# Kernel optimization log

Measured on AMD Instinct MI355X. Metric: run time of the kernel, lower is better.

The kernel has to match this reference:

```python
import jax, jax.numpy as jnp
import numpy as np

N_NODES = 100000
N_EDGES = 1600000
IN_DIM, HID, OUT = 128, 128, 64


def setup_inputs() -> dict:
    key = jax.random.key(0)
    ks = jax.random.split(key, 8)
    x = jax.random.normal(ks[0], (N_NODES, IN_DIM), dtype=jnp.float32)
    edge_index = jax.random.randint(ks[1], (2, N_EDGES), 0, N_NODES, dtype=jnp.int64)
    # Glorot-ish init for GCNConv linear weights (stored as [in, out]).
    W1 = jax.random.normal(ks[2], (IN_DIM, HID), dtype=jnp.float32) * (1.0 / np.sqrt(IN_DIM))
    b1 = jnp.zeros((HID,), dtype=jnp.float32)
    W2 = jax.random.normal(ks[3], (HID, HID), dtype=jnp.float32) * (1.0 / np.sqrt(HID))
    b2 = jnp.zeros((HID,), dtype=jnp.float32)
    W3 = jax.random.normal(ks[4], (HID, OUT), dtype=jnp.float32) * (1.0 / np.sqrt(HID))
    b3 = jnp.zeros((OUT,), dtype=jnp.float32)
    return {"x": x, "W1": W1, "b1": b1, "W2": W2, "b2": b2,
            "W3": W3, "b3": b3, "edge_index": edge_index}


def _gcn_norm(edge_index, num_nodes):
    # GCNConv default: add self loops, symmetric normalization D^{-1/2} A D^{-1/2}.
    loops = jnp.arange(num_nodes, dtype=edge_index.dtype)
    src = jnp.concatenate([edge_index[0], loops])
    dst = jnp.concatenate([edge_index[1], loops])
    deg = jax.ops.segment_sum(jnp.ones_like(dst, dtype=jnp.float32), dst,
                              num_segments=num_nodes)
    dinv = jnp.where(deg > 0, jax.lax.rsqrt(deg), 0.0)
    norm = dinv[src] * dinv[dst]  # [E + N]
    return src, dst, norm


def _gcn_conv(h, W, b, src, dst, norm, num_nodes):
    h = h @ W                                   # transform first (PyG GCNConv)
    msg = h[src] * norm[:, None]                # gather + scale
    agg = jax.ops.segment_sum(msg, dst, num_segments=num_nodes)  # scatter-add
    return agg + b


def _dropout(h, key, p=0.5):
    keep = jax.random.bernoulli(key, 1.0 - p, h.shape)
    return jnp.where(keep, h / (1.0 - p), 0.0)


def reference(x, W1, b1, W2, b2, W3, b3, edge_index):
    num_nodes = x.shape[0]
    src, dst, norm = _gcn_norm(edge_index, num_nodes)
    kd1, kd2 = jax.random.split(jax.random.key(42))
    h = jax.nn.relu(_gcn_conv(x, W1, b1, src, dst, norm, num_nodes))
    h = _dropout(h, kd1)
    h = jax.nn.relu(_gcn_conv(h, W2, b2, src, dst, norm, num_nodes))
    h = _dropout(h, kd2)
    return _gcn_conv(h, W3, b3, src, dst, norm, num_nodes)
```

## Files before the change

### kernel.cpp

```cpp
#include <hip/hip_runtime.h>
#include <stdint.h>

#define NN 100000
#define NE 1600000
#define NMASKW 400000
#define HIST_BLKS 6250
#define WSPL_BLKS 20

typedef float f4 __attribute__((ext_vector_type(4)));
typedef float f2 __attribute__((ext_vector_type(2)));
typedef unsigned short us4 __attribute__((ext_vector_type(4)));
typedef short s16x8 __attribute__((ext_vector_type(8)));

__device__ inline float bf2f(unsigned short u) {
  return __uint_as_float(((uint32_t)u) << 16);
}
__device__ inline unsigned short f2bf(float f) {
  uint32_t u = __float_as_uint(f);
  return (unsigned short)((u + 0x7fffu + ((u >> 16) & 1u)) >> 16);
}
__device__ inline float lo16(uint32_t q) { return __uint_as_float(q << 16); }
__device__ inline float hi16(uint32_t q) { return __uint_as_float(q & 0xffff0000u); }

__host__ __device__ inline void threefry2x32(uint32_t k0, uint32_t k1,
                                             uint32_t x0, uint32_t x1,
                                             uint32_t* y0, uint32_t* y1) {
  uint32_t ks[3] = {k0, k1, k0 ^ k1 ^ 0x1BD11BDAu};
  x0 += ks[0]; x1 += ks[1];
  const uint32_t R[2][4] = {{13u, 15u, 26u, 6u}, {17u, 29u, 16u, 24u}};
#pragma unroll
  for (int i = 0; i < 5; ++i) {
#pragma unroll
    for (int j = 0; j < 4; ++j) {
      uint32_t r = R[i & 1][j];
      x0 += x1;
      x1 = (x1 << r) | (x1 >> (32u - r));
      x1 ^= x0;
    }
    x0 += ks[(i + 1) % 3];
    x1 += ks[(i + 2) % 3] + (uint32_t)(i + 1);
  }
  *y0 = x0; *y1 = x1;
}

__device__ inline uint32_t tf_bits32(uint32_t k0, uint32_t k1, uint32_t idx) {
  uint32_t a, b;
  threefry2x32(k0, k1, 0u, idx, &a, &b);
  return a ^ b;
}

__global__ __launch_bounds__(256) void k_histmask(
    const int* __restrict__ ei, uint32_t* __restrict__ cnt,
    int* __restrict__ slot, uint32_t* __restrict__ m1, uint32_t* __restrict__ m2,
    uint32_t k10, uint32_t k11, uint32_t k20, uint32_t k21) {
  int b = blockIdx.x;
  int q = b / 5, r = b % 5;
  if (r < 4) {
    int e = (q * 4 + r) * 256 + threadIdx.x;
    if (e < NE) {
      int d = ei[NE + e];
      slot[e] = (int)atomicAdd(&cnt[d], 1u);
    }
  } else {
    int t = q * 256 + threadIdx.x;
    if (t < NMASKW) {
      uint32_t base = (uint32_t)t * 32u;
      uint32_t w1 = 0, w2 = 0;
#pragma unroll 4
      for (int j = 0; j < 32; ++j) {
        w1 |= (tf_bits32(k10, k11, base + j) >> 31) << j;
        w2 |= (tf_bits32(k20, k21, base + j) >> 31) << j;
      }
      m1[t] = w1;
      m2[t] = w2;
    }
  }
}

__global__ __launch_bounds__(256) void k_scan1(const uint32_t* __restrict__ cnt,
                                               uint32_t* __restrict__ rpp,
                                               uint32_t* __restrict__ bsum,
                                               float* __restrict__ dinv) {
  __shared__ uint32_t sh[256];
  int t = threadIdx.x;
  int base = blockIdx.x * 1024 + t * 4;
  uint32_t v[4];
  uint32_t s = 0;
#pragma unroll
  for (int i = 0; i < 4; ++i) {
    int idx = base + i;
    v[i] = (idx < NN) ? cnt[idx] : 0u;
    if (idx < NN) dinv[idx] = 1.0f / sqrtf((float)(v[i] + 1u));
    s += v[i];
  }
  sh[t] = s;
  __syncthreads();
  for (int off = 1; off < 256; off <<= 1) {
    uint32_t x = sh[t];
    if (t >= off) x += sh[t - off];
    __syncthreads();
    sh[t] = x;
    __syncthreads();
  }
  uint32_t run = (t > 0) ? sh[t - 1] : 0u;
  if (t == 255) bsum[blockIdx.x] = sh[255];
#pragma unroll
  for (int i = 0; i < 4; ++i) {
    int idx = base + i;
    if (idx < NN) rpp[idx] = run;
    run += v[i];
  }
}

__global__ __launch_bounds__(128) void k_scan2(const uint32_t* __restrict__ bsum,
                                               uint32_t* __restrict__ bsumP,
                                               uint32_t* __restrict__ rpp, int nb) {
  __shared__ uint32_t sh[128];
  int t = threadIdx.x;
  uint32_t v = (t < nb) ? bsum[t] : 0u;
  sh[t] = v;
  __syncthreads();
  for (int off = 1; off < 128; off <<= 1) {
    uint32_t x = sh[t];
    if (t >= off) x += sh[t - off];
    __syncthreads();
    sh[t] = x;
    __syncthreads();
  }
  uint32_t excl = (t > 0) ? sh[t - 1] : 0u;
  if (t < nb) bsumP[t] = excl;
  if (t == nb - 1) rpp[NN] = (uint32_t)NE - excl;
}

__global__ __launch_bounds__(256) void k_scatwsplit(
    const int* __restrict__ ei, const uint32_t* __restrict__ rpp,
    const uint32_t* __restrict__ bsumP,
    const int* __restrict__ slot, const float* __restrict__ dinv,
    uint2* __restrict__ e2,
    const float* __restrict__ W1, const float* __restrict__ W2,
    const float* __restrict__ W3,
    unsigned short* __restrict__ w1h, unsigned short* __restrict__ w1l,
    unsigned short* __restrict__ w2h, unsigned short* __restrict__ w2l,
    unsigned short* __restrict__ w3h, unsigned short* __restrict__ w3l) {
  int b = blockIdx.x;
  if (b < WSPL_BLKS) {
    int bb = b * 4 + (threadIdx.x >> 6);
    int lane = threadIdx.x & 63;
    const float* W; unsigned short *H, *L; int dout, j0;
    if (bb < 32)      { W = W1; H = w1h; L = w1l; dout = 128; j0 = bb; }
    else if (bb < 64) { W = W2; H = w2h; L = w2l; dout = 128; j0 = bb - 32; }
    else              { W = W3; H = w3h; L = w3l; dout = 64;  j0 = bb - 64; }
    int kk = j0 & 3;
    int ct = j0 >> 2;
    int kbase = kk * 32 + (lane >> 4) * 8;
    int col = ct * 16 + (lane & 15);
    us4 h0, h1, l0, l1;
#pragma unroll
    for (int j = 0; j < 4; ++j) {
      float v = W[(size_t)(kbase + j) * dout + col];
      h0[j] = f2bf(v);
      l0[j] = f2bf(v - bf2f(h0[j]));
      float v2 = W[(size_t)(kbase + 4 + j) * dout + col];
      h1[j] = f2bf(v2);
      l1[j] = f2bf(v2 - bf2f(h1[j]));
    }
    size_t o = ((size_t)j0 * 64 + lane) * 8;
    *(us4*)(H + o) = h0; *(us4*)(H + o + 4) = h1;
    *(us4*)(L + o) = l0; *(us4*)(L + o + 4) = l1;
  } else {
    int e = (b - WSPL_BLKS) * 256 + threadIdx.x;
    if (e < NE) {
      int s = ei[e];
      int d = ei[NE + e];
      float w = dinv[s] * dinv[d];
      uint2 rec;
      rec.x = (uint32_t)s;
      rec.y = __float_as_uint(w);
      uint32_t pos = rpp[d] + bsumP[(uint32_t)d >> 10] + (uint32_t)slot[e];
      e2[pos] = rec;
    }
  }
}

__global__ __launch_bounds__(256) void k_gemm1(
    const float* __restrict__ A, const unsigned short* __restrict__ Wh,
    const unsigned short* __restrict__ Wl, unsigned short* __restrict__ C) {
  constexpr int NT = 8;
  const int w = threadIdx.x >> 6;
  const int lane = threadIdx.x & 63;
  const int row0 = blockIdx.x * 128 + w * 32;
  const int aoff = (lane >> 4) * 8;
  s16x8 afh[2][4], afl[2][4];
#pragma unroll
  for (int g = 0; g < 2; ++g) {
    int ar = row0 + g * 16 + (lane & 15);
    if (ar >= NN) ar = NN - 1;
#pragma unroll
    for (int kk = 0; kk < 4; ++kk) {
      f4 v0 = *(const f4*)(A + (size_t)ar * 128 + kk * 32 + aoff);
      f4 v1 = *(const f4*)(A + (size_t)ar * 128 + kk * 32 + aoff + 4);
#pragma unroll
      for (int j = 0; j < 4; ++j) {
        unsigned short h = f2bf(v0[j]);
        afh[g][kk][j] = (short)h;
        afl[g][kk][j] = (short)f2bf(v0[j] - bf2f(h));
        unsigned short h2 = f2bf(v1[j]);
        afh[g][kk][j + 4] = (short)h2;
        afl[g][kk][j + 4] = (short)f2bf(v1[j] - bf2f(h2));
      }
    }
  }
  f4 acc[2][NT];
#pragma unroll
  for (int g = 0; g < 2; ++g)
#pragma unroll
    for (int t = 0; t < NT; ++t) acc[g][t] = (f4){0.f, 0.f, 0.f, 0.f};
#pragma unroll
  for (int ct = 0; ct < NT; ++ct) {
#pragma unroll
    for (int kk = 0; kk < 4; ++kk) {
      size_t bo = ((size_t)(ct * 4 + kk) * 64 + lane) * 8;
      s16x8 bh = *(const s16x8*)(Wh + bo);
      s16x8 bl = *(const s16x8*)(Wl + bo);
#pragma unroll
      for (int g = 0; g < 2; ++g) {
        acc[g][ct] = __builtin_amdgcn_mfma_f32_16x16x32_bf16(afh[g][kk], bh, acc[g][ct], 0, 0, 0);
        acc[g][ct] = __builtin_amdgcn_mfma_f32_16x16x32_bf16(afh[g][kk], bl, acc[g][ct], 0, 0, 0);
        acc[g][ct] = __builtin_amdgcn_mfma_f32_16x16x32_bf16(afl[g][kk], bh, acc[g][ct], 0, 0, 0);
      }
    }
  }
  const int cbase = lane & 15;
#pragma unroll
  for (int g = 0; g < 2; ++g) {
    const int rbase = row0 + g * 16 + (lane >> 4) * 4;
#pragma unroll
    for (int ct = 0; ct < NT; ++ct) {
#pragma unroll
      for (int r = 0; r < 4; ++r) {
        int gr = rbase + r;
        if (gr < NN) C[(size_t)gr * 128 + ct * 16 + cbase] = f2bf(acc[g][ct][r]);
      }
    }
  }
}

template <int DOUT>
__global__ __launch_bounds__(256) void k_gemm_mfma(
    const unsigned short* __restrict__ Ah, const unsigned short* __restrict__ Al,
    const unsigned short* __restrict__ Wh, const unsigned short* __restrict__ Wl,
    unsigned short* __restrict__ C) {
  constexpr int NT = DOUT / 16;
  const int w = threadIdx.x >> 6;
  const int lane = threadIdx.x & 63;
  const int row0 = blockIdx.x * 128 + w * 32;
  const int aoff = (lane >> 4) * 8;
  s16x8 afh[2][4], afl[2][4];
#pragma unroll
  for (int g = 0; g < 2; ++g) {
    int ar = row0 + g * 16 + (lane & 15);
    if (ar >= NN) ar = NN - 1;
#pragma unroll
    for (int kk = 0; kk < 4; ++kk) {
      afh[g][kk] = *(const s16x8*)(Ah + (size_t)ar * 128 + kk * 32 + aoff);
      afl[g][kk] = *(const s16x8*)(Al + (size_t)ar * 128 + kk * 32 + aoff);
    }
  }
  f4 acc[2][NT];
#pragma unroll
  for (int g = 0; g < 2; ++g)
#pragma unroll
    for (int t = 0; t < NT; ++t) acc[g][t] = (f4){0.f, 0.f, 0.f, 0.f};
#pragma unroll
  for (int ct = 0; ct < NT; ++ct) {
#pragma unroll
    for (int kk = 0; kk < 4; ++kk) {
      size_t bo = ((size_t)(ct * 4 + kk) * 64 + lane) * 8;
      s16x8 bh = *(const s16x8*)(Wh + bo);
      s16x8 bl = *(const s16x8*)(Wl + bo);
#pragma unroll
      for (int g = 0; g < 2; ++g) {
        acc[g][ct] = __builtin_amdgcn_mfma_f32_16x16x32_bf16(afh[g][kk], bh, acc[g][ct], 0, 0, 0);
        acc[g][ct] = __builtin_amdgcn_mfma_f32_16x16x32_bf16(afh[g][kk], bl, acc[g][ct], 0, 0, 0);
        acc[g][ct] = __builtin_amdgcn_mfma_f32_16x16x32_bf16(afl[g][kk], bh, acc[g][ct], 0, 0, 0);
      }
    }
  }
  const int cbase = lane & 15;
#pragma unroll
  for (int g = 0; g < 2; ++g) {
    const int rbase = row0 + g * 16 + (lane >> 4) * 4;
#pragma unroll
    for (int ct = 0; ct < NT; ++ct) {
#pragma unroll
      for (int r = 0; r < 4; ++r) {
        int gr = rbase + r;
        if (gr < NN) C[(size_t)gr * DOUT + ct * 16 + cbase] = f2bf(acc[g][ct][r]);
      }
    }
  }
}

__global__ __launch_bounds__(256) void k_agg_mid(
    const unsigned short* __restrict__ hb, const uint32_t* __restrict__ rpp,
    const uint32_t* __restrict__ bsumP,
    const uint2* __restrict__ e2, const float* __restrict__ dinv,
    const float* __restrict__ bias, const uint32_t* __restrict__ mask,
    unsigned short* __restrict__ oh, unsigned short* __restrict__ ol) {
  int wid = __builtin_amdgcn_readfirstlane(blockIdx.x * 4 + (threadIdx.x >> 6));
  if (wid >= NN) return;
  const int lane = threadIdx.x & 63;
  const int q = lane >> 4;
  const int fl = lane & 15;
  const uint32_t beg = rpp[wid] + bsumP[(uint32_t)wid >> 10];
  const uint32_t end = rpp[wid + 1] + bsumP[(uint32_t)(wid + 1) >> 10];
  const float dv = dinv[wid];
  const float sn = dv * dv;
  const char* hbase = (const char*)hb;
  f2 acc[4];
#pragma unroll
  for (int j = 0; j < 4; ++j) acc[j] = (f2){0.f, 0.f};

#define ACC4(g, wv)                                                        \
  {                                                                        \
    f2 wv2 = {wv, wv};                                                     \
    f2 h0 = {lo16(g.x), hi16(g.x)}; acc[0] += wv2 * h0;                    \
    f2 h1 = {lo16(g.y), hi16(g.y)}; acc[1] += wv2 * h1;                    \
    f2 h2 = {lo16(g.z), hi16(g.z)}; acc[2] += wv2 * h2;                    \
    f2 h3 = {lo16(g.w), hi16(g.w)}; acc[3] += wv2 * h3;                    \
  }

  uint32_t u = beg;
  for (; u + 16 <= end; u += 16) {
    uint2 r0 = e2[u + q];
    uint2 r1 = e2[u + 4 + q];
    uint2 r2 = e2[u + 8 + q];
    uint2 r3 = e2[u + 12 + q];
    uint4 g0 = *(const uint4*)(hbase + ((size_t)r0.x << 8) + fl * 16);
    uint4 g1 = *(const uint4*)(hbase + ((size_t)r1.x << 8) + fl * 16);
    uint4 g2 = *(const uint4*)(hbase + ((size_t)r2.x << 8) + fl * 16);
    uint4 g3 = *(const uint4*)(hbase + ((size_t)r3.x << 8) + fl * 16);
    float w0 = __uint_as_float(r0.y), w1 = __uint_as_float(r1.y);
    float w2 = __uint_as_float(r2.y), w3 = __uint_as_float(r3.y);
    ACC4(g0, w0); ACC4(g1, w1); ACC4(g2, w2); ACC4(g3, w3);
  }
  for (; u < end; u += 4) {
    uint32_t idx = u + (uint32_t)q;
    uint32_t cidx = idx < end ? idx : end - 1u;
    uint2 r = e2[cidx];
    float w = (idx < end) ? __uint_as_float(r.y) : 0.f;
    uint4 g = *(const uint4*)(hbase + ((size_t)r.x << 8) + fl * 16);
    ACC4(g, w);
  }
#undef ACC4

#pragma unroll
  for (int j = 0; j < 4; ++j) {
    acc[j][0] += __shfl_xor(acc[j][0], 16);
    acc[j][1] += __shfl_xor(acc[j][1], 16);
    acc[j][0] += __shfl_xor(acc[j][0], 32);
    acc[j][1] += __shfl_xor(acc[j][1], 32);
  }

  uint4 qs = *(const uint4*)(hbase + ((size_t)(uint32_t)wid << 8) + fl * 16);
  f2 snv = {sn, sn};
  f2 h0 = {lo16(qs.x), hi16(qs.x)};
  f2 h1 = {lo16(qs.y), hi16(qs.y)};
  f2 h2 = {lo16(qs.z), hi16(qs.z)};
  f2 h3 = {lo16(qs.w), hi16(qs.w)};
  acc[0] += snv * h0; acc[1] += snv * h1;
  acc[2] += snv * h2; acc[3] += snv * h3;
#pragma unroll
  for (int j = 0; j < 4; ++j) acc[j] += *(const f2*)(bias + fl * 8 + 2 * j);

  uint32_t mw = mask[(uint32_t)wid * 4u + (uint32_t)(fl >> 2)];
  uint32_t bb = (uint32_t)((fl & 3) * 8);
  uint32_t hw[4], lw[4];
#pragma unroll
  for (int j = 0; j < 4; ++j) {
    float a0 = fmaxf(acc[j][0], 0.f);
    float a1 = fmaxf(acc[j][1], 0.f);
    a0 = ((mw >> (bb + 2 * j)) & 1u) ? 0.f : a0 * 2.f;
    a1 = ((mw >> (bb + 2 * j + 1)) & 1u) ? 0.f : a1 * 2.f;
    unsigned short hh0 = f2bf(a0), hh1 = f2bf(a1);
    unsigned short g0 = f2bf(a0 - bf2f(hh0)), g1 = f2bf(a1 - bf2f(hh1));
    hw[j] = (uint32_t)hh0 | ((uint32_t)hh1 << 16);
    lw[j] = (uint32_t)g0 | ((uint32_t)g1 << 16);
  }
  if (q == 0) {
    uint4 v = {hw[0], hw[1], hw[2], hw[3]};
    *(uint4*)(oh + (size_t)(uint32_t)wid * 128 + fl * 8) = v;
  } else if (q == 1) {
    uint4 v = {lw[0], lw[1], lw[2], lw[3]};
    *(uint4*)(ol + (size_t)(uint32_t)wid * 128 + fl * 8) = v;
  }
}

__global__ __launch_bounds__(256) void k_agg_final(
    const unsigned short* __restrict__ hb, const uint32_t* __restrict__ rpp,
    const uint32_t* __restrict__ bsumP,
    const uint2* __restrict__ e2, const float* __restrict__ dinv,
    const float* __restrict__ bias, float* __restrict__ out) {
  int wid = __builtin_amdgcn_readfirstlane(blockIdx.x * 4 + (threadIdx.x >> 6));
  if (wid >= NN) return;
  const int lane = threadIdx.x & 63;
  const int q = lane >> 4;
  const int fl = lane & 15;
  const uint32_t beg = rpp[wid] + bsumP[(uint32_t)wid >> 10];
  const uint32_t end = rpp[wid + 1] + bsumP[(uint32_t)(wid + 1) >> 10];
  const float dv = dinv[wid];
  const float sn = dv * dv;
  const char* hbase = (const char*)hb;
  f2 acc[2];
  acc[0] = (f2){0.f, 0.f};
  acc[1] = (f2){0.f, 0.f};

#define ACC2(g, wv)                                                        \
  {                                                                        \
    f2 wv2 = {wv, wv};                                                     \
    f2 h0 = {lo16(g.x), hi16(g.x)}; acc[0] += wv2 * h0;                    \
    f2 h1 = {lo16(g.y), hi16(g.y)}; acc[1] += wv2 * h1;                    \
  }

  uint32_t u = beg;
  for (; u + 16 <= end; u += 16) {
    uint2 r0 = e2[u + q];
    uint2 r1 = e2[u + 4 + q];
    uint2 r2 = e2[u + 8 + q];
    uint2 r3 = e2[u + 12 + q];
    uint2 g0 = *(const uint2*)(hbase + ((size_t)r0.x << 7) + fl * 8);
    uint2 g1 = *(const uint2*)(hbase + ((size_t)r1.x << 7) + fl * 8);
    uint2 g2 = *(const uint2*)(hbase + ((size_t)r2.x << 7) + fl * 8);
    uint2 g3 = *(const uint2*)(hbase + ((size_t)r3.x << 7) + fl * 8);
    float w0 = __uint_as_float(r0.y), w1 = __uint_as_float(r1.y);
    float w2 = __uint_as_float(r2.y), w3 = __uint_as_float(r3.y);
    ACC2(g0, w0); ACC2(g1, w1); ACC2(g2, w2); ACC2(g3, w3);
  }
  for (; u < end; u += 4) {
    uint32_t idx = u + (uint32_t)q;
    uint32_t cidx = idx < end ? idx : end - 1u;
    uint2 r = e2[cidx];
    float w = (idx < end) ? __uint_as_float(r.y) : 0.f;
    uint2 g = *(const uint2*)(hbase + ((size_t)r.x << 7) + fl * 8);
    ACC2(g, w);
  }
#undef ACC2

#pragma unroll
  for (int j = 0; j < 2; ++j) {
    acc[j][0] += __shfl_xor(acc[j][0], 16);
    acc[j][1] += __shfl_xor(acc[j][1], 16);
    acc[j][0] += __shfl_xor(acc[j][0], 32);
    acc[j][1] += __shfl_xor(acc[j][1], 32);
  }

  uint2 qs = *(const uint2*)(hbase + ((size_t)(uint32_t)wid << 7) + fl * 8);
  f2 snv = {sn, sn};
  f2 h0 = {lo16(qs.x), hi16(qs.x)};
  f2 h1 = {lo16(qs.y), hi16(qs.y)};
  acc[0] += snv * h0;
  acc[1] += snv * h1;
  acc[0] += *(const f2*)(bias + fl * 4);
  acc[1] += *(const f2*)(bias + fl * 4 + 2);
  if (q == 0) {
    f4 v = {acc[0][0], acc[0][1], acc[1][0], acc[1][1]};
    *(f4*)(out + (size_t)(uint32_t)wid * 64 + fl * 4) = v;
  }
}

extern "C" void kernel_launch(void* const* d_in, const int* in_sizes, int n_in,
                              void* d_out, int out_size, void* d_ws, size_t ws_size,
                              hipStream_t stream) {
  (void)in_sizes; (void)n_in; (void)out_size; (void)ws_size;
  const float* x  = (const float*)d_in[0];
  const float* W1 = (const float*)d_in[1];
  const float* b1 = (const float*)d_in[2];
  const float* W2 = (const float*)d_in[3];
  const float* b2 = (const float*)d_in[4];
  const float* W3 = (const float*)d_in[5];
  const float* b3 = (const float*)d_in[6];
  const int* ei   = (const int*)d_in[7];
  float* out = (float*)d_out;

  char* p = (char*)d_ws;
  auto alloc = [&](size_t bytes) -> void* {
    void* r = (void*)p;
    p += (bytes + 255) & ~(size_t)255;
    return r;
  };
  uint32_t* cnt   = (uint32_t*)alloc((size_t)NN * 4);
  float*    dinv  = (float*)alloc((size_t)NN * 4);
  uint32_t* rpp   = (uint32_t*)alloc((size_t)(NN + 1) * 4);
  uint32_t* bsum  = (uint32_t*)alloc(1024);
  uint32_t* bsumP = (uint32_t*)alloc(1024);
  int*      slot  = (int*)alloc((size_t)NE * 4);
  uint2*    e2    = (uint2*)alloc((size_t)NE * 8);
  uint32_t* m1    = (uint32_t*)alloc((size_t)NMASKW * 4);
  uint32_t* m2    = (uint32_t*)alloc((size_t)NMASKW * 4);
  unsigned short* ah = (unsigned short*)alloc((size_t)NN * 128 * 2);
  unsigned short* al = (unsigned short*)alloc((size_t)NN * 128 * 2);
  unsigned short* hb = (unsigned short*)alloc((size_t)NN * 128 * 2);
  unsigned short* w1h = (unsigned short*)alloc(32 * 64 * 8 * 2);
  unsigned short* w1l = (unsigned short*)alloc(32 * 64 * 8 * 2);
  unsigned short* w2h = (unsigned short*)alloc(32 * 64 * 8 * 2);
  unsigned short* w2l = (unsigned short*)alloc(32 * 64 * 8 * 2);
  unsigned short* w3h = (unsigned short*)alloc(16 * 64 * 8 * 2);
  unsigned short* w3l = (unsigned short*)alloc(16 * 64 * 8 * 2);

  uint32_t kd1a, kd1b, kd2a, kd2b;
  threefry2x32(0u, 42u, 0u, 0u, &kd1a, &kd1b);
  threefry2x32(0u, 42u, 0u, 1u, &kd2a, &kd2b);

  const int gbScan = (NN + 1023) / 1024;
  const int gbGemm = (NN + 127) / 128;
  const int gbAgg = (NN + 3) / 4;

  hipMemsetAsync(cnt, 0, (size_t)NN * 4, stream);
  k_histmask<<<8000, 256, 0, stream>>>(ei, cnt, slot, m1, m2, kd1a, kd1b, kd2a, kd2b);
  k_scan1<<<gbScan, 256, 0, stream>>>(cnt, rpp, bsum, dinv);
  k_scan2<<<1, 128, 0, stream>>>(bsum, bsumP, rpp, gbScan);
  k_scatwsplit<<<WSPL_BLKS + HIST_BLKS, 256, 0, stream>>>(
      ei, rpp, bsumP, slot, dinv, e2, W1, W2, W3, w1h, w1l, w2h, w2l, w3h, w3l);

  k_gemm1<<<gbGemm, 256, 0, stream>>>(x, w1h, w1l, hb);
  k_agg_mid<<<gbAgg, 256, 0, stream>>>(hb, rpp, bsumP, e2, dinv, b1, m1, ah, al);
  k_gemm_mfma<128><<<gbGemm, 256, 0, stream>>>(ah, al, w2h, w2l, hb);
  k_agg_mid<<<gbAgg, 256, 0, stream>>>(hb, rpp, bsumP, e2, dinv, b2, m2, ah, al);
  k_gemm_mfma<64><<<gbGemm, 256, 0, stream>>>(ah, al, w3h, w3l, hb);
  k_agg_final<<<gbAgg, 256, 0, stream>>>(hb, rpp, bsumP, e2, dinv, b3, out);
}
```

Baseline: 392.0 us.

## Build CSR with per-chunk LDS histograms instead of global atomics

Replaces the global-atomic degree histogram and per-edge slot array with LDS-privatized histograms over 64 edge chunks and 4 node ranges, stored as packed 16-bit counts. A per-chunk prefix over those counts is computed in the scan kernel, and the scatter re-derives each edge's rank with LDS atomics, which removes the memset, the slot buffer and the global atomic contention. The dropout mask generation now runs in a separate kernel alongside the weight split. Each chunk is read four times (once per node range) and the scan kernel now reads 64 chunk counts per node. Edge order within a destination is no longer deterministic, which could perturb float summation order.

```diff
diff --git a/kernel.cpp b/kernel.cpp
--- a/kernel.cpp
+++ b/kernel.cpp
@@ -4,7 +4,11 @@
 #define NN 100000
 #define NE 1600000
 #define NMASKW 400000
-#define HIST_BLKS 6250
+#define NRANGE 4
+#define RSZ 25000
+#define NCHUNK 64
+#define ECHUNK 25000
+#define MASK_BLKS 1563
 #define WSPL_BLKS 20
 
 typedef float f4 __attribute__((ext_vector_type(4)));
@@ -49,50 +53,56 @@
   return a ^ b;
 }
 
-__global__ __launch_bounds__(256) void k_histmask(
-    const int* __restrict__ ei, uint32_t* __restrict__ cnt,
-    int* __restrict__ slot, uint32_t* __restrict__ m1, uint32_t* __restrict__ m2,
-    uint32_t k10, uint32_t k11, uint32_t k20, uint32_t k21) {
-  int b = blockIdx.x;
-  int q = b / 5, r = b % 5;
-  if (r < 4) {
-    int e = (q * 4 + r) * 256 + threadIdx.x;
-    if (e < NE) {
-      int d = ei[NE + e];
-      slot[e] = (int)atomicAdd(&cnt[d], 1u);
-    }
-  } else {
-    int t = q * 256 + threadIdx.x;
-    if (t < NMASKW) {
-      uint32_t base = (uint32_t)t * 32u;
-      uint32_t w1 = 0, w2 = 0;
-#pragma unroll 4
-      for (int j = 0; j < 32; ++j) {
-        w1 |= (tf_bits32(k10, k11, base + j) >> 31) << j;
-        w2 |= (tf_bits32(k20, k21, base + j) >> 31) << j;
-      }
-      m1[t] = w1;
-      m2[t] = w2;
-    }
-  }
-}
-
-__global__ __launch_bounds__(256) void k_scan1(const uint32_t* __restrict__ cnt,
+__global__ __launch_bounds__(256) void k_hist_lds(const int* __restrict__ ei,
+                                                  unsigned short* __restrict__ hc) {
+  __shared__ uint32_t h[RSZ / 2];
+  const int r = blockIdx.x & (NRANGE - 1);
+  const int c = blockIdx.x >> 2;
+  const int lo = r * RSZ;
+  for (int i = threadIdx.x; i < RSZ / 2; i += 256) h[i] = 0u;
+  __syncthreads();
+  const int* dp = ei + NE + c * ECHUNK;
+  for (int i = threadIdx.x * 4; i < ECHUNK; i += 1024) {
+    int4 d4 = *(const int4*)(dp + i);
+#define CNT(dd)                                                           \
+    {                                                                     \
+      uint32_t x = (uint32_t)((dd) - lo);                                 \
+      if (x < (uint32_t)RSZ)                                              \
+        atomicAdd(&h[x >> 1], (x & 1u) ? 0x10000u : 1u);                  \
+    }
+    CNT(d4.x); CNT(d4.y); CNT(d4.z); CNT(d4.w);
+#undef CNT
+  }
+  __syncthreads();
+  uint32_t* dst = (uint32_t*)(hc + (size_t)c * NN + lo);
+  for (int i = threadIdx.x; i < RSZ / 2; i += 256) dst[i] = h[i];
+}
+
+__global__ __launch_bounds__(256) void k_scan1(const unsigned short* __restrict__ hc,
+                                               unsigned short* __restrict__ cp,
                                                uint32_t* __restrict__ rpp,
                                                uint32_t* __restrict__ bsum,
                                                float* __restrict__ dinv) {
   __shared__ uint32_t sh[256];
   int t = threadIdx.x;
-  int base = blockIdx.x * 1024 + t * 4;
-  uint32_t v[4];
-  uint32_t s = 0;
-#pragma unroll
-  for (int i = 0; i < 4; ++i) {
-    int idx = base + i;
-    v[i] = (idx < NN) ? cnt[idx] : 0u;
-    if (idx < NN) dinv[idx] = 1.0f / sqrtf((float)(v[i] + 1u));
-    s += v[i];
-  }
+  int n0 = blockIdx.x * 1024 + t * 4;
+  uint32_t v0 = 0, v1 = 0, v2 = 0, v3 = 0;
+  if (n0 < NN) {
+    for (int c = 0; c < NCHUNK; ++c) {
+      const uint32_t* src = (const uint32_t*)(hc + (size_t)c * NN + n0);
+      uint32_t a = src[0], b = src[1];
+      uint32_t* d = (uint32_t*)(cp + (size_t)c * NN + n0);
+      d[0] = (v0 & 0xffffu) | (v1 << 16);
+      d[1] = (v2 & 0xffffu) | (v3 << 16);
+      v0 += a & 0xffffu; v1 += a >> 16;
+      v2 += b & 0xffffu; v3 += b >> 16;
+    }
+    dinv[n0]     = 1.0f / sqrtf((float)(v0 + 1u));
+    dinv[n0 + 1] = 1.0f / sqrtf((float)(v1 + 1u));
+    dinv[n0 + 2] = 1.0f / sqrtf((float)(v2 + 1u));
+    dinv[n0 + 3] = 1.0f / sqrtf((float)(v3 + 1u));
+  }
+  uint32_t s = v0 + v1 + v2 + v3;
   sh[t] = s;
   __syncthreads();
   for (int off = 1; off < 256; off <<= 1) {
@@ -104,11 +114,11 @@
   }
   uint32_t run = (t > 0) ? sh[t - 1] : 0u;
   if (t == 255) bsum[blockIdx.x] = sh[255];
-#pragma unroll
-  for (int i = 0; i < 4; ++i) {
-    int idx = base + i;
-    if (idx < NN) rpp[idx] = run;
-    run += v[i];
+  if (n0 < NN) {
+    rpp[n0] = run;       run += v0;
+    rpp[n0 + 1] = run;   run += v1;
+    rpp[n0 + 2] = run;   run += v2;
+    rpp[n0 + 3] = run;
   }
 }
 
@@ -132,11 +142,9 @@
   if (t == nb - 1) rpp[NN] = (uint32_t)NE - excl;
 }
 
-__global__ __launch_bounds__(256) void k_scatwsplit(
-    const int* __restrict__ ei, const uint32_t* __restrict__ rpp,
-    const uint32_t* __restrict__ bsumP,
-    const int* __restrict__ slot, const float* __restrict__ dinv,
-    uint2* __restrict__ e2,
+__global__ __launch_bounds__(256) void k_maskwsplit(
+    uint32_t* __restrict__ m1, uint32_t* __restrict__ m2,
+    uint32_t k10, uint32_t k11, uint32_t k20, uint32_t k21,
     const float* __restrict__ W1, const float* __restrict__ W2,
     const float* __restrict__ W3,
     unsigned short* __restrict__ w1h, unsigned short* __restrict__ w1l,
@@ -168,17 +176,53 @@
     *(us4*)(H + o) = h0; *(us4*)(H + o + 4) = h1;
     *(us4*)(L + o) = l0; *(us4*)(L + o + 4) = l1;
   } else {
-    int e = (b - WSPL_BLKS) * 256 + threadIdx.x;
-    if (e < NE) {
-      int s = ei[e];
-      int d = ei[NE + e];
-      float w = dinv[s] * dinv[d];
-      uint2 rec;
-      rec.x = (uint32_t)s;
-      rec.y = __float_as_uint(w);
-      uint32_t pos = rpp[d] + bsumP[(uint32_t)d >> 10] + (uint32_t)slot[e];
-      e2[pos] = rec;
-    }
+    int t = (b - WSPL_BLKS) * 256 + threadIdx.x;
+    if (t < NMASKW) {
+      uint32_t base = (uint32_t)t * 32u;
+      uint32_t w1 = 0, w2 = 0;
+#pragma unroll 4
+      for (int j = 0; j < 32; ++j) {
+        w1 |= (tf_bits32(k10, k11, base + j) >> 31) << j;
+        w2 |= (tf_bits32(k20, k21, base + j) >> 31) << j;
+      }
+      m1[t] = w1;
+      m2[t] = w2;
+    }
+  }
+}
+
+__global__ __launch_bounds__(256) void k_scat_lds(
+    const int* __restrict__ ei, const uint32_t* __restrict__ rpp,
+    const uint32_t* __restrict__ bsumP, const unsigned short* __restrict__ cp,
+    const float* __restrict__ dinv, uint2* __restrict__ e2) {
+  __shared__ uint32_t rk[RSZ / 2];
+  const int r = blockIdx.x & (NRANGE - 1);
+  const int c = blockIdx.x >> 2;
+  const int lo = r * RSZ;
+  for (int i = threadIdx.x; i < RSZ / 2; i += 256) rk[i] = 0u;
+  __syncthreads();
+  const int* sp = ei + c * ECHUNK;
+  const int* dp = ei + NE + c * ECHUNK;
+  const unsigned short* cpc = cp + (size_t)c * NN;
+  for (int i = threadIdx.x * 4; i < ECHUNK; i += 1024) {
+    int4 s4 = *(const int4*)(sp + i);
+    int4 d4 = *(const int4*)(dp + i);
+#define SCAT(ss, dd)                                                      \
+    {                                                                     \
+      uint32_t x = (uint32_t)((dd) - lo);                                 \
+      if (x < (uint32_t)RSZ) {                                            \
+        uint32_t old = atomicAdd(&rk[x >> 1], (x & 1u) ? 0x10000u : 1u);  \
+        uint32_t rank = (x & 1u) ? (old >> 16) : (old & 0xffffu);         \
+        uint32_t pos = rpp[dd] + bsumP[(uint32_t)(dd) >> 10] +            \
+                       (uint32_t)cpc[dd] + rank;                          \
+        uint2 rec;                                                        \
+        rec.x = (uint32_t)(ss);                                           \
+        rec.y = __float_as_uint(dinv[ss] * dinv[dd]);                     \
+        e2[pos] = rec;                                                    \
+      }                                                                   \
+    }
+    SCAT(s4.x, d4.x); SCAT(s4.y, d4.y); SCAT(s4.z, d4.z); SCAT(s4.w, d4.w);
+#undef SCAT
   }
 }
 
@@ -488,12 +532,10 @@
     p += (bytes + 255) & ~(size_t)255;
     return r;
   };
-  uint32_t* cnt   = (uint32_t*)alloc((size_t)NN * 4);
   float*    dinv  = (float*)alloc((size_t)NN * 4);
   uint32_t* rpp   = (uint32_t*)alloc((size_t)(NN + 1) * 4);
   uint32_t* bsum  = (uint32_t*)alloc(1024);
   uint32_t* bsumP = (uint32_t*)alloc(1024);
-  int*      slot  = (int*)alloc((size_t)NE * 4);
   uint2*    e2    = (uint2*)alloc((size_t)NE * 8);
   uint32_t* m1    = (uint32_t*)alloc((size_t)NMASKW * 4);
   uint32_t* m2    = (uint32_t*)alloc((size_t)NMASKW * 4);
@@ -507,6 +549,9 @@
   unsigned short* w3h = (unsigned short*)alloc(16 * 64 * 8 * 2);
   unsigned short* w3l = (unsigned short*)alloc(16 * 64 * 8 * 2);
 
+  unsigned short* hc = ah;
+  unsigned short* cp = al;
+
   uint32_t kd1a, kd1b, kd2a, kd2b;
   threefry2x32(0u, 42u, 0u, 0u, &kd1a, &kd1b);
   threefry2x32(0u, 42u, 0u, 1u, &kd2a, &kd2b);
@@ -515,12 +560,13 @@
   const int gbGemm = (NN + 127) / 128;
   const int gbAgg = (NN + 3) / 4;
 
-  hipMemsetAsync(cnt, 0, (size_t)NN * 4, stream);
-  k_histmask<<<8000, 256, 0, stream>>>(ei, cnt, slot, m1, m2, kd1a, kd1b, kd2a, kd2b);
-  k_scan1<<<gbScan, 256, 0, stream>>>(cnt, rpp, bsum, dinv);
+  k_hist_lds<<<NRANGE * NCHUNK, 256, 0, stream>>>(ei, hc);
+  k_maskwsplit<<<WSPL_BLKS + MASK_BLKS, 256, 0, stream>>>(
+      m1, m2, kd1a, kd1b, kd2a, kd2b, W1, W2, W3,
+      w1h, w1l, w2h, w2l, w3h, w3l);
+  k_scan1<<<gbScan, 256, 0, stream>>>(hc, cp, rpp, bsum, dinv);
   k_scan2<<<1, 128, 0, stream>>>(bsum, bsumP, rpp, gbScan);
-  k_scatwsplit<<<WSPL_BLKS + HIST_BLKS, 256, 0, stream>>>(
-      ei, rpp, bsumP, slot, dinv, e2, W1, W2, W3, w1h, w1l, w2h, w2l, w3h, w3l);
+  k_scat_lds<<<NRANGE * NCHUNK, 256, 0, stream>>>(ei, rpp, bsumP, cp, dinv, e2);
 
   k_gemm1<<<gbGemm, 256, 0, stream>>>(x, w1h, w1l, hb);
   k_agg_mid<<<gbAgg, 256, 0, stream>>>(hb, rpp, bsumP, e2, dinv, b1, m1, ah, al);
```

Measured after the change: 413.2 us. 1.05x slower.
